# Optimization experiments

Measured on AMD Instinct MI355X. Metric: run time of the kernel, lower is better.

## Reference

```python
import jax, jax.numpy as jnp
import numpy as np

N_NODES = 20000
N_EDGES = 200000
N_GRAPHS = 128
EMB = 256
N_LAYERS = 4
NUM_ELEMENTS = 84
RBF_DIM = 10
RBF_CUTOFF = 8.0


def setup_inputs() -> dict:
    key = jax.random.key(0)
    ks = jax.random.split(key, 20)
    inp = {
        'x': jax.random.randint(ks[0], (N_NODES, 1), 0, NUM_ELEMENTS, dtype=jnp.int64) if jax.config.read('jax_enable_x64') else jax.random.randint(ks[0], (N_NODES, 1), 0, NUM_ELEMENTS).astype(jnp.int32),
        'src': jax.random.randint(ks[1], (N_EDGES,), 0, N_NODES).astype(jnp.int32),
        'dst': jax.random.randint(ks[2], (N_EDGES,), 0, N_NODES).astype(jnp.int32),
        'e': jax.random.uniform(ks[3], (N_EDGES, 1), dtype=jnp.float32) * RBF_CUTOFF,
        'i': jnp.sort(jax.random.randint(ks[4], (N_NODES,), 0, N_GRAPHS)).astype(jnp.int32),
    }
    s_emb = 1.0 / np.sqrt(EMB)
    # element embedding table
    inp['emb_table'] = jax.random.normal(ks[5], (NUM_ELEMENTS, EMB), jnp.float32) * s_emb
    # dense_e applied to RBF expansion
    inp['We'] = jax.random.normal(ks[6], (RBF_DIM, EMB), jnp.float32) * (1.0 / np.sqrt(RBF_DIM))
    inp['be'] = jnp.zeros((EMB,), jnp.float32)
    # CGCNN-style gated message passing layers (stacked over layers)
    def w(k):
        return jax.random.normal(k, (N_LAYERS, EMB, EMB), jnp.float32) * s_emb
    inp['Wg_x'] = w(ks[7]); inp['Wg_n'] = w(ks[8]); inp['Wg_e'] = w(ks[9])
    inp['bg'] = jnp.zeros((N_LAYERS, EMB), jnp.float32)
    inp['Wf_x'] = w(ks[10]); inp['Wf_n'] = w(ks[11]); inp['Wf_e'] = w(ks[12])
    inp['bf'] = jnp.zeros((N_LAYERS, EMB), jnp.float32)
    # dense_n: embedding -> 12
    inp['Wn'] = jax.random.normal(ks[13], (EMB, 12), jnp.float32) * s_emb
    inp['bn'] = jnp.zeros((12,), jnp.float32)
    return inp


def _rbf_expand(d):
    # Gaussian radial basis expansion of scalar distances: [E] -> [E, RBF_DIM]
    centers = jnp.linspace(0.0, RBF_CUTOFF, RBF_DIM, dtype=d.dtype)
    width = centers[1] - centers[0]
    return jnp.exp(-(((d[:, None] - centers) / width) ** 2))


def reference(x, src, dst, e, i, emb_table, We, be, Wg_x, Wg_n, Wg_e, bg,
              Wf_x, Wf_n, Wf_e, bf, Wn, bn):
    xn = emb_table[x[:, 0]]                     # [N, EMB] element embedding
    ef = _rbf_expand(e[:, 0]) @ We + be         # [E, EMB] edge features
    for l in range(N_LAYERS):
        h_i = xn[dst]                           # receiver node features [E, EMB]
        h_j = xn[src]                           # sender node features   [E, EMB]
        # gate/filter computed as split matmuls (equivalent to Dense on concat)
        zg = h_i @ Wg_x[l] + h_j @ Wg_n[l] + ef @ Wg_e[l] + bg[l]
        zf = h_i @ Wf_x[l] + h_j @ Wf_n[l] + ef @ Wf_e[l] + bf[l]
        msg = jax.nn.sigmoid(zg) * jax.nn.softplus(zf)   # [E, EMB]
        agg = jax.ops.segment_sum(msg, dst, num_segments=N_NODES)
        xn = agg + xn                           # residual add (in model call)
    xs = xn @ Wn + bn                           # [N, 12]
    sums = jax.ops.segment_sum(xs, i, num_segments=N_GRAPHS)
    cnts = jax.ops.segment_sum(jnp.ones((xs.shape[0], 1), xs.dtype), i,
                               num_segments=N_GRAPHS)
    out = sums / jnp.maximum(cnts, 1.0)         # global average pool per graph
    return out.reshape(N_GRAPHS, 3, 4)
```

## Files before the change

### kernel.cpp

```cpp
#include <hip/hip_runtime.h>
#include <hip/hip_bf16.h>
#include <math.h>

#define NN   20000
#define NE   200000
#define NG   128
#define EMBD 256
#define NL   4
#define RBFD 10
#define RBFP 12
#define GSPL 8

typedef __attribute__((ext_vector_type(8))) short bf16x8;
typedef __attribute__((ext_vector_type(4))) float f32x4;
typedef __attribute__((ext_vector_type(2))) float f32x2;

__device__ __forceinline__ f32x4 unpk(uint2 u) {
  f32x4 r;
  r.x = __uint_as_float(u.x << 16);
  r.y = __uint_as_float(u.x & 0xffff0000u);
  r.z = __uint_as_float(u.y << 16);
  r.w = __uint_as_float(u.y & 0xffff0000u);
  return r;
}


__global__ void k_embed(const int* __restrict__ x, const float* __restrict__ emb,
                        float* __restrict__ xn, __hip_bfloat16* __restrict__ xnb) {
  int idx = blockIdx.x * blockDim.x + threadIdx.x;
  if (idx >= NN * (EMBD / 4)) return;
  int n  = idx >> 6;
  int c4 = (idx & 63) << 2;
  float4 v = *(const float4*)(emb + (size_t)x[n] * EMBD + c4);
  *(float4*)(xn + (size_t)n * EMBD + c4) = v;
  __hip_bfloat16* xb = xnb + (size_t)n * EMBD + c4;
  xb[0] = __float2bfloat16(v.x); xb[1] = __float2bfloat16(v.y);
  xb[2] = __float2bfloat16(v.z); xb[3] = __float2bfloat16(v.w);
}

__global__ void k_wsmall(const float* __restrict__ We, const float* __restrict__ be,
                         const float* __restrict__ Wge, const float* __restrict__ bg,
                         const float* __restrict__ Wfe, const float* __restrict__ bf,
                         float* __restrict__ weff, float* __restrict__ beff) {
  int tid = blockIdx.x * blockDim.x + threadIdx.x;
  const int WPER = RBFD * EMBD;
  if (tid < NL * 2 * WPER) {
    int l  = tid / (2 * WPER);
    int r  = tid % (2 * WPER);
    int gf = r / WPER;
    int r2 = r % WPER;
    int k = r2 / EMBD, c = r2 % EMBD;
    const float* W = (gf == 0 ? Wge : Wfe) + (size_t)l * EMBD * EMBD;
    float s = 0.f;
    for (int j = 0; j < EMBD; ++j) s += We[k * EMBD + j] * W[(size_t)j * EMBD + c];
    weff[tid] = s;
  } else {
    int t2 = tid - NL * 2 * WPER;
    if (t2 >= NL * 2 * EMBD) return;
    int l  = t2 / (2 * EMBD);
    int r  = t2 % (2 * EMBD);
    int gf = r / EMBD, c = r % EMBD;
    const float* W = (gf == 0 ? Wge : Wfe) + (size_t)l * EMBD * EMBD;
    const float* b = (gf == 0 ? bg : bf) + (size_t)l * EMBD;
    float s = b[c];
    for (int j = 0; j < EMBD; ++j) s += be[j] * W[(size_t)j * EMBD + c];
    beff[t2] = s;
  }
}

__global__ __launch_bounds__(256) void k_wprep(
    const float* __restrict__ Wgx, const float* __restrict__ Wfx,
    const float* __restrict__ Wgn, const float* __restrict__ Wfn,
    __hip_bfloat16* __restrict__ WT) {
  __shared__ float T[64][65];
  int lq = blockIdx.x; int l = lq >> 2, q = lq & 3;
  const float* W = (q == 0 ? Wgx : q == 1 ? Wfx : q == 2 ? Wgn : Wfn) + (size_t)l * 65536;
  int t = blockIdx.y;
  int k0 = (t & 3) * 64, c0 = (t >> 2) * 64;
  #pragma unroll
  for (int i = 0; i < 16; ++i) {
    int idx = threadIdx.x + i * 256;
    int r = idx >> 6, c = idx & 63;
    T[r][c] = W[(size_t)(k0 + r) * 256 + c0 + c];
  }
  __syncthreads();
  __hip_bfloat16* out = WT + ((size_t)lq * 256) * 256;
  #pragma unroll
  for (int i = 0; i < 16; ++i) {
    int idx = threadIdx.x + i * 256;
    int r = idx >> 6, c = idx & 63;
    out[(size_t)(c0 + r) * 256 + k0 + c] = __float2bfloat16(T[c][r]);
  }
}


__global__ void k_hist(const int* __restrict__ dst, int* __restrict__ cnt) {
  int e = blockIdx.x * blockDim.x + threadIdx.x;
  if (e >= NE) return;
  atomicAdd(&cnt[dst[e]], 1);
}

__global__ __launch_bounds__(1024) void k_scan(const int* __restrict__ cnt,
                                               int* __restrict__ roff,
                                               int* __restrict__ cursor) {
  __shared__ int part[1024];
  const int t = threadIdx.x;
  const int CH = 20;
  int base = t * CH;
  int loc[CH];
  int s = 0;
  #pragma unroll
  for (int i = 0; i < CH; ++i) {
    int idx = base + i;
    int v = (idx < NN) ? cnt[idx] : 0;
    loc[i] = s;
    s += v;
  }
  part[t] = s;
  __syncthreads();
  for (int off = 1; off < 1024; off <<= 1) {
    int v = (t >= off) ? part[t - off] : 0;
    __syncthreads();
    part[t] += v;
    __syncthreads();
  }
  int chunkbase = (t == 0) ? 0 : part[t - 1];
  #pragma unroll
  for (int i = 0; i < CH; ++i) {
    int idx = base + i;
    if (idx < NN) {
      int v = chunkbase + loc[i];
      roff[idx] = v;
      cursor[idx] = v;
    }
  }
  if (t == 1023) roff[NN] = part[1023];
}

__global__ void k_scatter(const int* __restrict__ src, const int* __restrict__ dst,
                          const float* __restrict__ edist,
                          int* __restrict__ cursor,
                          int* __restrict__ src_s, float* __restrict__ rbf_s) {
  int e = blockIdx.x * blockDim.x + threadIdx.x;
  if (e >= NE) return;
  int d = dst[e];
  int p = atomicAdd(&cursor[d], 1);
  src_s[p] = src[e];
  float dd = edist[e];
  const float width = 8.0f / 9.0f;
  float r[RBFD];
  #pragma unroll
  for (int k = 0; k < RBFD; ++k) {
    float t = (dd - (float)k * width) / width;
    r[k] = __expf(-t * t);
  }
  float* rp = rbf_s + (size_t)p * RBFP;
  *(float4*)(rp + 0) = make_float4(r[0], r[1], r[2], r[3]);
  *(float4*)(rp + 4) = make_float4(r[4], r[5], r[6], r[7]);
  *(float4*)(rp + 8) = make_float4(r[8], r[9], 0.f, 0.f);
}


__global__ __launch_bounds__(256) void k_nodemm(
    const __hip_bfloat16* __restrict__ xnb, const __hip_bfloat16* __restrict__ WTl,
    __hip_bfloat16* __restrict__ Yb) {
  __shared__ unsigned short As[128 * 32];
  __shared__ unsigned short Bs[128 * 32];
  const int tid = threadIdx.x;
  const int lane = tid & 63;
  const int wave = tid >> 6;
  const int row0 = blockIdx.x << 7;
  const int by = blockIdx.y;
  const int col0 = by << 7;
  const int q = col0 >> 8;
  const int cb = col0 & 255;
  const unsigned short* xb = (const unsigned short*)xnb;
  const unsigned short* Wb = (const unsigned short*)WTl + ((size_t)q * 256 + cb) * 256;
  const int wr = (wave >> 1) << 6;
  const int wc = (wave & 1) << 6;
  f32x4 acc[4][4] = {};

  for (int k0 = 0; k0 < 256; k0 += 32) {
    #pragma unroll
    for (int h = 0; h < 2; ++h) {
      int c = tid + (h << 8);
      int r = c >> 2, s = c & 3;
      int sw = s ^ ((r >> 1) & 3);
      int ga = row0 + r; if (ga > NN - 1) ga = NN - 1;
      *(bf16x8*)(&As[r * 32 + sw * 8]) =
          *(const bf16x8*)(xb + (size_t)ga * 256 + k0 + s * 8);
      *(bf16x8*)(&Bs[r * 32 + sw * 8]) =
          *(const bf16x8*)(Wb + (size_t)r * 256 + k0 + s * 8);
    }
    __syncthreads();
    bf16x8 af[4], bfr[4];
    const int rsel = lane & 15, ksl = lane >> 4;
    #pragma unroll
    for (int m = 0; m < 4; ++m) {
      int r = wr + m * 16 + rsel;
      int sw = ksl ^ ((r >> 1) & 3);
      af[m] = *(const bf16x8*)(&As[r * 32 + sw * 8]);
    }
    #pragma unroll
    for (int n = 0; n < 4; ++n) {
      int r = wc + n * 16 + rsel;
      int sw = ksl ^ ((r >> 1) & 3);
      bfr[n] = *(const bf16x8*)(&Bs[r * 32 + sw * 8]);
    }
    #pragma unroll
    for (int m = 0; m < 4; ++m)
      #pragma unroll
      for (int n = 0; n < 4; ++n)
        acc[m][n] = __builtin_amdgcn_mfma_f32_16x16x32_bf16(af[m], bfr[n], acc[m][n], 0, 0, 0);
    __syncthreads();
  }

  const int crow = (lane >> 4) << 2;
  const int ccol = lane & 15;
  #pragma unroll
  for (int m = 0; m < 4; ++m)
    #pragma unroll
    for (int j = 0; j < 4; ++j) {
      int gr = row0 + wr + m * 16 + crow + j;
      if (gr < NN) {
        #pragma unroll
        for (int n = 0; n < 4; ++n)
          Yb[(size_t)gr * 1024 + col0 + wc + n * 16 + ccol] = __float2bfloat16(acc[m][n][j]);
      }
    }
}

__device__ __forceinline__ float fast_sigmoid(float z) {
  return __builtin_amdgcn_rcpf(1.0f + __expf(-z));
}
__device__ __forceinline__ float fast_softplus(float z) {
  return fmaxf(z, 0.0f) + __logf(1.0f + __expf(-fabsf(z)));
}

__global__ __launch_bounds__(256, 3) void k_agg(
    const __hip_bfloat16* __restrict__ Yb, const int* __restrict__ roff,
    const int* __restrict__ src_s, const float* __restrict__ rbf_s,
    const float* __restrict__ weff, const float* __restrict__ beff,
    float* __restrict__ xn, __hip_bfloat16* __restrict__ xnb, int layer) {
  const int wave = threadIdx.x >> 6, lane = threadIdx.x & 63;
  const int c4 = lane << 2;
  const int n = blockIdx.x * 4 + wave;
  if (n >= NN) return;
  const int jb = __builtin_amdgcn_readfirstlane(roff[n]);
  const int deg = roff[n + 1] - jb;

  const float* wg_g = weff + (size_t)layer * 2 * RBFD * EMBD + c4;
  const float* wf_g = wg_g + RBFD * EMBD;
  f32x4 wg[RBFD], wf[RBFD];
  #pragma unroll
  for (int k = 0; k < RBFD; ++k) {
    wg[k] = *(const f32x4*)(wg_g + k * EMBD);
    wf[k] = *(const f32x4*)(wf_g + k * EMBD);
  }
  const float* bb = beff + (size_t)layer * 2 * EMBD + c4;
  f32x4 bgv = *(const f32x4*)(bb);
  f32x4 bfv = *(const f32x4*)(bb + EMBD);

  const unsigned short* yrow = (const unsigned short*)Yb + (size_t)n * 1024 + c4;
  f32x4 bg = bgv + unpk(*(const uint2*)(yrow));
  f32x4 bf = bfv + unpk(*(const uint2*)(yrow + 256));

  f32x4 macc = {};
  if (deg > 0) {
    int sv = (lane < deg) ? src_s[jb + lane] : 0;
    const unsigned short* Ysrc = (const unsigned short*)Yb + c4 + 512;
    int s0 = __shfl(sv, 0, 64);
    uint2 pa = *(const uint2*)(Ysrc + (size_t)s0 * 1024);
    uint2 pf = *(const uint2*)(Ysrc + (size_t)s0 * 1024 + 256);
    const float* rp0 = rbf_s + (size_t)jb * RBFP;
    f32x4 r03 = *(const f32x4*)(rp0);
    f32x4 r47 = *(const f32x4*)(rp0 + 4);
    f32x2 r89 = *(const f32x2*)(rp0 + 8);
    for (int i = 0; i < deg; ++i) {
      uint2 na = pa, nf2 = pf;
      f32x4 n03 = r03, n47 = r47; f32x2 n89 = r89;
      if (i + 1 < deg) {
        int sn = (i + 1 < 64) ? __shfl(sv, i + 1, 64) : src_s[jb + i + 1];
        na  = *(const uint2*)(Ysrc + (size_t)sn * 1024);
        nf2 = *(const uint2*)(Ysrc + (size_t)sn * 1024 + 256);
        const float* rp = rbf_s + (size_t)(jb + i + 1) * RBFP;
        n03 = *(const f32x4*)(rp);
        n47 = *(const f32x4*)(rp + 4);
        n89 = *(const f32x2*)(rp + 8);
      }
      f32x4 zg = bg + unpk(pa);
      f32x4 zf = bf + unpk(pf);
      zg += r03.x * wg[0]; zf += r03.x * wf[0];
      zg += r03.y * wg[1]; zf += r03.y * wf[1];
      zg += r03.z * wg[2]; zf += r03.z * wf[2];
      zg += r03.w * wg[3]; zf += r03.w * wf[3];
      zg += r47.x * wg[4]; zf += r47.x * wf[4];
      zg += r47.y * wg[5]; zf += r47.y * wf[5];
      zg += r47.z * wg[6]; zf += r47.z * wf[6];
      zg += r47.w * wg[7]; zf += r47.w * wf[7];
      zg += r89.x * wg[8]; zf += r89.x * wf[8];
      zg += r89.y * wg[9]; zf += r89.y * wf[9];
      macc.x += fast_sigmoid(zg.x) * fast_softplus(zf.x);
      macc.y += fast_sigmoid(zg.y) * fast_softplus(zf.y);
      macc.z += fast_sigmoid(zg.z) * fast_softplus(zf.z);
      macc.w += fast_sigmoid(zg.w) * fast_softplus(zf.w);
      pa = na; pf = nf2; r03 = n03; r47 = n47; r89 = n89;
    }
  }
  float4 xv = *(const float4*)(xn + (size_t)n * EMBD + c4);
  xv.x += macc.x; xv.y += macc.y; xv.z += macc.z; xv.w += macc.w;
  *(float4*)(xn + (size_t)n * EMBD + c4) = xv;
  __hip_bfloat16* xbp = xnb + (size_t)n * EMBD + c4;
  xbp[0] = __float2bfloat16(xv.x); xbp[1] = __float2bfloat16(xv.y);
  xbp[2] = __float2bfloat16(xv.z); xbp[3] = __float2bfloat16(xv.w);
}


__global__ __launch_bounds__(256) void k_gsum(
    const float* __restrict__ xn, const int* __restrict__ gi,
    float* __restrict__ gpart, float* __restrict__ gcnt) {
  const int g = blockIdx.x, p = blockIdx.y;
  int lo = 0, hi = NN;
  while (lo < hi) { int m = (lo + hi) >> 1; if (gi[m] < g) lo = m + 1; else hi = m; }
  int lo2 = lo, hi2 = NN;
  while (lo2 < hi2) { int m = (lo2 + hi2) >> 1; if (gi[m] < g + 1) lo2 = m + 1; else hi2 = m; }
  const int cntv = lo2 - lo;
  const int r0 = lo + (cntv * p) / GSPL;
  const int r1 = lo + (cntv * (p + 1)) / GSPL;
  const int c = threadIdx.x;
  float acc = 0.f;
  for (int r = r0; r < r1; ++r) acc += xn[(size_t)r * EMBD + c];
  gpart[((size_t)g * GSPL + p) * EMBD + c] = acc;
  if (p == 0 && c == 0) gcnt[g] = (float)cntv;
}

__global__ __launch_bounds__(256) void k_final(
    const float* __restrict__ gpart, const float* __restrict__ gcnt,
    const float* __restrict__ Wn, const float* __restrict__ bn,
    float* __restrict__ out) {
  __shared__ float s[EMBD];
  const int g = blockIdx.x;
  const int c = threadIdx.x;
  float v = 0.f;
  #pragma unroll
  for (int p = 0; p < GSPL; ++p) v += gpart[((size_t)g * GSPL + p) * EMBD + c];
  s[c] = v;
  __syncthreads();
  if (c < 12) {
    float acc = 0.f;
    for (int k = 0; k < EMBD; ++k) acc += s[k] * Wn[k * 12 + c];
    float cv = gcnt[g];
    out[g * 12 + c] = (cv > 0.f) ? acc / cv + bn[c] : 0.f;
  }
}


extern "C" void kernel_launch(void* const* d_in, const int* in_sizes, int n_in,
                              void* d_out, int out_size, void* d_ws, size_t ws_size,
                              hipStream_t stream) {
  const int*   x   = (const int*)d_in[0];
  const int*   src = (const int*)d_in[1];
  const int*   dst = (const int*)d_in[2];
  const float* e   = (const float*)d_in[3];
  const int*   gi  = (const int*)d_in[4];
  const float* emb = (const float*)d_in[5];
  const float* We  = (const float*)d_in[6];
  const float* be  = (const float*)d_in[7];
  const float* Wgx = (const float*)d_in[8];
  const float* Wgn = (const float*)d_in[9];
  const float* Wge = (const float*)d_in[10];
  const float* bg  = (const float*)d_in[11];
  const float* Wfx = (const float*)d_in[12];
  const float* Wfn = (const float*)d_in[13];
  const float* Wfe = (const float*)d_in[14];
  const float* bf  = (const float*)d_in[15];
  const float* Wn  = (const float*)d_in[16];
  const float* bn  = (const float*)d_in[17];
  float* out = (float*)d_out;

  char* ws = (char*)d_ws;
  size_t off = 0;
  auto alloc = [&](size_t bytes) {
    void* p = ws + off;
    off += (bytes + 255) & ~(size_t)255;
    return p;
  };
  float*           xn    = (float*)alloc((size_t)NN * EMBD * 4);
  __hip_bfloat16*  xnb   = (__hip_bfloat16*)alloc((size_t)NN * EMBD * 2);
  __hip_bfloat16*  Yb    = (__hip_bfloat16*)alloc((size_t)NN * 1024 * 2);
  float*           rbf_s = (float*)alloc((size_t)NE * RBFP * 4);
  int*             src_s = (int*)alloc((size_t)NE * 4);
  int*             cnt   = (int*)alloc((size_t)NN * 4);
  int*             roff  = (int*)alloc((size_t)(NN + 1) * 4);
  int*             curs  = (int*)alloc((size_t)NN * 4);
  float*           weff  = (float*)alloc((size_t)NL * 2 * RBFD * EMBD * 4);
  float*           beff  = (float*)alloc((size_t)NL * 2 * EMBD * 4);
  __hip_bfloat16*  WT    = (__hip_bfloat16*)alloc((size_t)NL * 4 * 256 * 256 * 2);
  float*           gpart = (float*)alloc((size_t)NG * GSPL * EMBD * 4);
  float*           gcnt  = (float*)alloc((size_t)NG * 4);
  (void)ws_size; (void)in_sizes; (void)n_in; (void)out_size;

  hipMemsetAsync(cnt, 0, (size_t)NN * 4, stream);

  k_embed<<<(NN * (EMBD / 4) + 255) / 256, 256, 0, stream>>>(x, emb, xn, xnb);
  k_wsmall<<<(NL * 2 * (RBFD + 1) * EMBD + 255) / 256, 256, 0, stream>>>(
      We, be, Wge, bg, Wfe, bf, weff, beff);
  k_wprep<<<dim3(NL * 4, 16), 256, 0, stream>>>(Wgx, Wfx, Wgn, Wfn, WT);
  k_hist<<<(NE + 255) / 256, 256, 0, stream>>>(dst, cnt);
  k_scan<<<1, 1024, 0, stream>>>(cnt, roff, curs);
  k_scatter<<<(NE + 255) / 256, 256, 0, stream>>>(src, dst, e, curs, src_s, rbf_s);

  dim3 mmgrid((NN + 127) / 128, 8);
  for (int l = 0; l < NL; ++l) {
    k_nodemm<<<mmgrid, 256, 0, stream>>>(xnb, WT + (size_t)l * 4 * 65536, Yb);
    k_agg<<<(NN + 3) / 4, 256, 0, stream>>>(Yb, roff, src_s, rbf_s, weff, beff, xn, xnb, l);
  }
  k_gsum<<<dim3(NG, GSPL), 256, 0, stream>>>(xn, gi, gpart, gcnt);
  k_final<<<NG, 256, 0, stream>>>(gpart, gcnt, Wn, bn, out);
}
```

Measured before the change: 567.1 us.

## Replace per-edge RBF projection with interpolated distance lookup table

Precomputes, per layer, a 1025-bin table of the RBF-projected edge contribution (gate and filter, bias included) over distance, then linearly interpolates it in the aggregation kernel instead of doing 20 vector FMAs against register-held weights. The scatter now stores a single scaled distance per edge instead of 12 RBF floats. The aggregation kernel also becomes persistent (grid-stride over nodes), raises its occupancy hint, and broadcasts per-edge indices with readlane while dropping the software prefetch. The table adds about 8 MB of memory traffic plus gather loads, and interpolation introduces approximation error in the edge features.

```diff
diff --git a/kernel.cpp b/kernel.cpp
--- a/kernel.cpp
+++ b/kernel.cpp
@@ -8,14 +8,14 @@
 #define EMBD 256
 #define NL   4
 #define RBFD 10
-#define RBFP 12
+#define TBINS 1024
+#define NWAVE 8192
 #define GSPL 8
 
 typedef __attribute__((ext_vector_type(8))) short bf16x8;
 typedef __attribute__((ext_vector_type(4))) float f32x4;
-typedef __attribute__((ext_vector_type(2))) float f32x2;
-
-__device__ __forceinline__ f32x4 unpk(uint2 u) {
+
+__device__ __forceinline__ f32x4 up4(uint2 u) {
   f32x4 r;
   r.x = __uint_as_float(u.x << 16);
   r.y = __uint_as_float(u.x & 0xffff0000u);
@@ -68,6 +68,27 @@
   }
 }
 
+__global__ void k_table(const float* __restrict__ weff, const float* __restrict__ beff,
+                        float* __restrict__ tbl) {
+  int idx = blockIdx.x * blockDim.x + threadIdx.x;
+  if (idx >= NL * (TBINS + 1) * 512) return;
+  int l = idx / ((TBINS + 1) * 512);
+  int r = idx % ((TBINS + 1) * 512);
+  int bin = r >> 9;
+  int t = r & 511;
+  int gf = t >> 8, c = t & 255;
+  float d = (float)bin * (8.0f / (float)TBINS);
+  const float* w = weff + ((size_t)(l * 2 + gf) * RBFD) * EMBD + c;
+  float s = beff[(size_t)(l * 2 + gf) * EMBD + c];
+  const float width = 8.0f / 9.0f;
+  #pragma unroll
+  for (int k = 0; k < RBFD; ++k) {
+    float u = (d - (float)k * width) / width;
+    s += __expf(-u * u) * w[(size_t)k * EMBD];
+  }
+  tbl[idx] = s;
+}
+
 __global__ __launch_bounds__(256) void k_wprep(
     const float* __restrict__ Wgx, const float* __restrict__ Wfx,
     const float* __restrict__ Wgn, const float* __restrict__ Wfn,
@@ -140,24 +161,14 @@
 __global__ void k_scatter(const int* __restrict__ src, const int* __restrict__ dst,
                           const float* __restrict__ edist,
                           int* __restrict__ cursor,
-                          int* __restrict__ src_s, float* __restrict__ rbf_s) {
+                          int* __restrict__ src_s, float* __restrict__ db_s) {
   int e = blockIdx.x * blockDim.x + threadIdx.x;
   if (e >= NE) return;
   int d = dst[e];
   int p = atomicAdd(&cursor[d], 1);
   src_s[p] = src[e];
-  float dd = edist[e];
-  const float width = 8.0f / 9.0f;
-  float r[RBFD];
-  #pragma unroll
-  for (int k = 0; k < RBFD; ++k) {
-    float t = (dd - (float)k * width) / width;
-    r[k] = __expf(-t * t);
-  }
-  float* rp = rbf_s + (size_t)p * RBFP;
-  *(float4*)(rp + 0) = make_float4(r[0], r[1], r[2], r[3]);
-  *(float4*)(rp + 4) = make_float4(r[4], r[5], r[6], r[7]);
-  *(float4*)(rp + 8) = make_float4(r[8], r[9], 0.f, 0.f);
+  float dd = edist[e] * ((float)TBINS / 8.0f);
+  db_s[p] = fminf(fmaxf(dd, 0.0f), (float)TBINS - 0.001f);
 }
 
 
@@ -230,89 +241,89 @@
     }
 }
 
-__device__ __forceinline__ float fast_sigmoid(float z) {
-  return __builtin_amdgcn_rcpf(1.0f + __expf(-z));
-}
-__device__ __forceinline__ float fast_softplus(float z) {
-  return fmaxf(z, 0.0f) + __logf(1.0f + __expf(-fabsf(z)));
-}
-
-__global__ __launch_bounds__(256, 3) void k_agg(
+__device__ __forceinline__ float gate1(float zg, float zf) {
+  float sg = __builtin_amdgcn_rcpf(1.0f + __expf(-zg));
+  float sp = fmaxf(zf, 0.0f) + __logf(1.0f + __expf(-fabsf(zf)));
+  return sg * sp;
+}
+
+__global__ __launch_bounds__(256, 8) void k_agg(
     const __hip_bfloat16* __restrict__ Yb, const int* __restrict__ roff,
-    const int* __restrict__ src_s, const float* __restrict__ rbf_s,
-    const float* __restrict__ weff, const float* __restrict__ beff,
-    float* __restrict__ xn, __hip_bfloat16* __restrict__ xnb, int layer) {
+    const int* __restrict__ src_s, const float* __restrict__ db_s,
+    const float* __restrict__ tblL,
+    float* __restrict__ xn, __hip_bfloat16* __restrict__ xnb) {
   const int wave = threadIdx.x >> 6, lane = threadIdx.x & 63;
   const int c4 = lane << 2;
-  const int n = blockIdx.x * 4 + wave;
-  if (n >= NN) return;
-  const int jb = __builtin_amdgcn_readfirstlane(roff[n]);
-  const int deg = roff[n + 1] - jb;
-
-  const float* wg_g = weff + (size_t)layer * 2 * RBFD * EMBD + c4;
-  const float* wf_g = wg_g + RBFD * EMBD;
-  f32x4 wg[RBFD], wf[RBFD];
-  #pragma unroll
-  for (int k = 0; k < RBFD; ++k) {
-    wg[k] = *(const f32x4*)(wg_g + k * EMBD);
-    wf[k] = *(const f32x4*)(wf_g + k * EMBD);
-  }
-  const float* bb = beff + (size_t)layer * 2 * EMBD + c4;
-  f32x4 bgv = *(const f32x4*)(bb);
-  f32x4 bfv = *(const f32x4*)(bb + EMBD);
-
-  const unsigned short* yrow = (const unsigned short*)Yb + (size_t)n * 1024 + c4;
-  f32x4 bg = bgv + unpk(*(const uint2*)(yrow));
-  f32x4 bf = bfv + unpk(*(const uint2*)(yrow + 256));
-
-  f32x4 macc = {};
-  if (deg > 0) {
-    int sv = (lane < deg) ? src_s[jb + lane] : 0;
-    const unsigned short* Ysrc = (const unsigned short*)Yb + c4 + 512;
-    int s0 = __shfl(sv, 0, 64);
-    uint2 pa = *(const uint2*)(Ysrc + (size_t)s0 * 1024);
-    uint2 pf = *(const uint2*)(Ysrc + (size_t)s0 * 1024 + 256);
-    const float* rp0 = rbf_s + (size_t)jb * RBFP;
-    f32x4 r03 = *(const f32x4*)(rp0);
-    f32x4 r47 = *(const f32x4*)(rp0 + 4);
-    f32x2 r89 = *(const f32x2*)(rp0 + 8);
-    for (int i = 0; i < deg; ++i) {
-      uint2 na = pa, nf2 = pf;
-      f32x4 n03 = r03, n47 = r47; f32x2 n89 = r89;
-      if (i + 1 < deg) {
-        int sn = (i + 1 < 64) ? __shfl(sv, i + 1, 64) : src_s[jb + i + 1];
-        na  = *(const uint2*)(Ysrc + (size_t)sn * 1024);
-        nf2 = *(const uint2*)(Ysrc + (size_t)sn * 1024 + 256);
-        const float* rp = rbf_s + (size_t)(jb + i + 1) * RBFP;
-        n03 = *(const f32x4*)(rp);
-        n47 = *(const f32x4*)(rp + 4);
-        n89 = *(const f32x2*)(rp + 8);
+  const int wid0 = blockIdx.x * 4 + wave;
+
+  for (int n = wid0; n < NN; n += NWAVE) {
+    const int jb   = __builtin_amdgcn_readfirstlane(roff[n]);
+    const int jend = __builtin_amdgcn_readfirstlane(roff[n + 1]);
+    const int deg = jend - jb;
+
+    const unsigned short* yrow = (const unsigned short*)Yb + (size_t)n * 1024 + c4;
+    f32x4 bgv = up4(*(const uint2*)(yrow));
+    f32x4 bfv = up4(*(const uint2*)(yrow + 256));
+
+    f32x4 m4 = {};
+    if (deg > 0) {
+      const int dcap = deg < 64 ? deg : 64;
+      int sv = 0; int bv = 0; int fv = 0;
+      if (lane < dcap) {
+        sv = src_s[jb + lane];
+        float db = db_s[jb + lane];
+        int b = (int)db;
+        bv = b;
+        fv = __float_as_int(db - (float)b);
       }
-      f32x4 zg = bg + unpk(pa);
-      f32x4 zf = bf + unpk(pf);
-      zg += r03.x * wg[0]; zf += r03.x * wf[0];
-      zg += r03.y * wg[1]; zf += r03.y * wf[1];
-      zg += r03.z * wg[2]; zf += r03.z * wf[2];
-      zg += r03.w * wg[3]; zf += r03.w * wf[3];
-      zg += r47.x * wg[4]; zf += r47.x * wf[4];
-      zg += r47.y * wg[5]; zf += r47.y * wf[5];
-      zg += r47.z * wg[6]; zf += r47.z * wf[6];
-      zg += r47.w * wg[7]; zf += r47.w * wf[7];
-      zg += r89.x * wg[8]; zf += r89.x * wf[8];
-      zg += r89.y * wg[9]; zf += r89.y * wf[9];
-      macc.x += fast_sigmoid(zg.x) * fast_softplus(zf.x);
-      macc.y += fast_sigmoid(zg.y) * fast_softplus(zf.y);
-      macc.z += fast_sigmoid(zg.z) * fast_softplus(zf.z);
-      macc.w += fast_sigmoid(zg.w) * fast_softplus(zf.w);
-      pa = na; pf = nf2; r03 = n03; r47 = n47; r89 = n89;
-    }
-  }
-  float4 xv = *(const float4*)(xn + (size_t)n * EMBD + c4);
-  xv.x += macc.x; xv.y += macc.y; xv.z += macc.z; xv.w += macc.w;
-  *(float4*)(xn + (size_t)n * EMBD + c4) = xv;
-  __hip_bfloat16* xbp = xnb + (size_t)n * EMBD + c4;
-  xbp[0] = __float2bfloat16(xv.x); xbp[1] = __float2bfloat16(xv.y);
-  xbp[2] = __float2bfloat16(xv.z); xbp[3] = __float2bfloat16(xv.w);
+      const unsigned short* Ysrc = (const unsigned short*)Yb + c4 + 512;
+      for (int i = 0; i < dcap; ++i) {
+        int sn = __builtin_amdgcn_readlane(sv, i);
+        int bn = __builtin_amdgcn_readlane(bv, i);
+        float fr = __int_as_float(__builtin_amdgcn_readlane(fv, i));
+        const unsigned short* ys = Ysrc + (size_t)sn * 1024;
+        uint2 pa = *(const uint2*)(ys);
+        uint2 pf = *(const uint2*)(ys + 256);
+        const float* tp = tblL + (size_t)bn * 512 + c4;
+        f32x4 t0g = *(const f32x4*)(tp);
+        f32x4 t0f = *(const f32x4*)(tp + 256);
+        f32x4 t1g = *(const f32x4*)(tp + 512);
+        f32x4 t1f = *(const f32x4*)(tp + 768);
+        f32x4 zg = bgv + up4(pa) + t0g + fr * (t1g - t0g);
+        f32x4 zf = bfv + up4(pf) + t0f + fr * (t1f - t0f);
+        m4.x += gate1(zg.x, zf.x);
+        m4.y += gate1(zg.y, zf.y);
+        m4.z += gate1(zg.z, zf.z);
+        m4.w += gate1(zg.w, zf.w);
+      }
+      for (int i = 64; i < deg; ++i) {
+        int sn = src_s[jb + i];
+        float db = db_s[jb + i];
+        int bn = (int)db;
+        float fr = db - (float)bn;
+        const unsigned short* ys = Ysrc + (size_t)sn * 1024;
+        uint2 pa = *(const uint2*)(ys);
+        uint2 pf = *(const uint2*)(ys + 256);
+        const float* tp = tblL + (size_t)bn * 512 + c4;
+        f32x4 t0g = *(const f32x4*)(tp);
+        f32x4 t0f = *(const f32x4*)(tp + 256);
+        f32x4 t1g = *(const f32x4*)(tp + 512);
+        f32x4 t1f = *(const f32x4*)(tp + 768);
+        f32x4 zg = bgv + up4(pa) + t0g + fr * (t1g - t0g);
+        f32x4 zf = bfv + up4(pf) + t0f + fr * (t1f - t0f);
+        m4.x += gate1(zg.x, zf.x);
+        m4.y += gate1(zg.y, zf.y);
+        m4.z += gate1(zg.z, zf.z);
+        m4.w += gate1(zg.w, zf.w);
+      }
+    }
+    float4 xv = *(const float4*)(xn + (size_t)n * EMBD + c4);
+    xv.x += m4.x; xv.y += m4.y; xv.z += m4.z; xv.w += m4.w;
+    *(float4*)(xn + (size_t)n * EMBD + c4) = xv;
+    __hip_bfloat16* xbp = xnb + (size_t)n * EMBD + c4;
+    xbp[0] = __float2bfloat16(xv.x); xbp[1] = __float2bfloat16(xv.y);
+    xbp[2] = __float2bfloat16(xv.z); xbp[3] = __float2bfloat16(xv.w);
+  }
 }
 
 
@@ -388,13 +399,14 @@
   float*           xn    = (float*)alloc((size_t)NN * EMBD * 4);
   __hip_bfloat16*  xnb   = (__hip_bfloat16*)alloc((size_t)NN * EMBD * 2);
   __hip_bfloat16*  Yb    = (__hip_bfloat16*)alloc((size_t)NN * 1024 * 2);
-  float*           rbf_s = (float*)alloc((size_t)NE * RBFP * 4);
+  float*           db_s  = (float*)alloc((size_t)NE * 4);
   int*             src_s = (int*)alloc((size_t)NE * 4);
   int*             cnt   = (int*)alloc((size_t)NN * 4);
   int*             roff  = (int*)alloc((size_t)(NN + 1) * 4);
   int*             curs  = (int*)alloc((size_t)NN * 4);
   float*           weff  = (float*)alloc((size_t)NL * 2 * RBFD * EMBD * 4);
   float*           beff  = (float*)alloc((size_t)NL * 2 * EMBD * 4);
+  float*           tbl   = (float*)alloc((size_t)NL * (TBINS + 1) * 512 * 4);
   __hip_bfloat16*  WT    = (__hip_bfloat16*)alloc((size_t)NL * 4 * 256 * 256 * 2);
   float*           gpart = (float*)alloc((size_t)NG * GSPL * EMBD * 4);
   float*           gcnt  = (float*)alloc((size_t)NG * 4);
@@ -405,15 +417,17 @@
   k_embed<<<(NN * (EMBD / 4) + 255) / 256, 256, 0, stream>>>(x, emb, xn, xnb);
   k_wsmall<<<(NL * 2 * (RBFD + 1) * EMBD + 255) / 256, 256, 0, stream>>>(
       We, be, Wge, bg, Wfe, bf, weff, beff);
+  k_table<<<(NL * (TBINS + 1) * 512 + 255) / 256, 256, 0, stream>>>(weff, beff, tbl);
   k_wprep<<<dim3(NL * 4, 16), 256, 0, stream>>>(Wgx, Wfx, Wgn, Wfn, WT);
   k_hist<<<(NE + 255) / 256, 256, 0, stream>>>(dst, cnt);
   k_scan<<<1, 1024, 0, stream>>>(cnt, roff, curs);
-  k_scatter<<<(NE + 255) / 256, 256, 0, stream>>>(src, dst, e, curs, src_s, rbf_s);
+  k_scatter<<<(NE + 255) / 256, 256, 0, stream>>>(src, dst, e, curs, src_s, db_s);
 
   dim3 mmgrid((NN + 127) / 128, 8);
   for (int l = 0; l < NL; ++l) {
     k_nodemm<<<mmgrid, 256, 0, stream>>>(xnb, WT + (size_t)l * 4 * 65536, Yb);
-    k_agg<<<(NN + 3) / 4, 256, 0, stream>>>(Yb, roff, src_s, rbf_s, weff, beff, xn, xnb, l);
+    k_agg<<<NWAVE / 4, 256, 0, stream>>>(
+        Yb, roff, src_s, db_s, tbl + (size_t)l * (TBINS + 1) * 512, xn, xnb);
   }
   k_gsum<<<dim3(NG, GSPL), 256, 0, stream>>>(xn, gi, gpart, gcnt);
   k_final<<<NG, 256, 0, stream>>>(gpart, gcnt, Wn, bn, out);
```

Result: faster. 490.4 us (-13.5%).
